# Optimization experiments

Hardware: AMD Instinct MI355X
Metric: run time of the kernel (lower is better)

Reference implementation:

```python
import jax, jax.numpy as jnp
import numpy as np

N, E, IN, HID, OUT, B = 50000, 800000, 128, 128, 64, 4096
EPS = 1e-5


def setup_inputs() -> dict:
    key = jax.random.key(0)
    ks = jax.random.split(key, 12)
    x = jax.random.normal(ks[0], (N, IN), jnp.float32)
    edge_index = jax.random.randint(ks[1], (2, E), 0, N, dtype=jnp.int32).astype(jnp.int64)
    target_index = jax.random.randint(ks[2], (B,), 0, N, dtype=jnp.int32).astype(jnp.int64)

    def lin(k, i, o):
        return jax.random.normal(k, (i, o), jnp.float32) * (1.0 / np.sqrt(i))

    return {
        'x': x, 'edge_index': edge_index, 'target_index': target_index,
        'W0': lin(ks[3], IN, HID), 'b0': jnp.zeros((HID,), jnp.float32),
        'W1': lin(ks[4], HID, HID), 'b1': jnp.zeros((HID,), jnp.float32),
        'W2': lin(ks[5], HID, HID), 'b2': jnp.zeros((HID,), jnp.float32),
        'g0': jnp.ones((HID,), jnp.float32), 'bt0': jnp.zeros((HID,), jnp.float32),
        'g1': jnp.ones((HID,), jnp.float32), 'bt1': jnp.zeros((HID,), jnp.float32),
        'f1w': lin(ks[6], HID, HID), 'f1b': jnp.zeros((HID,), jnp.float32),
        'f2w': lin(ks[7], HID, OUT), 'f2b': jnp.zeros((OUT,), jnp.float32),
    }


def _gcn_layer(h, W, b, src, dst, norm):
    # GCNConv: D^-1/2 (A+I) D^-1/2 (h W) + b  (self-loops already in src/dst)
    h = h @ W                                        # [N, out]
    msg = h[src] * norm[:, None]                     # [E+N, out]
    return jax.ops.segment_sum(msg, dst, num_segments=N) + b


def _batchnorm(h, g, bt):
    mu = jnp.mean(h, axis=0)
    var = jnp.mean((h - mu) ** 2, axis=0)            # biased, as torch BN
    return g * (h - mu) * jax.lax.rsqrt(var + EPS) + bt


def reference(x, edge_index, target_index, W0, b0, W1, b1, W2, b2,
              g0, bt0, g1, bt1, f1w, f1b, f2w, f2b):
    loop = jnp.arange(N, dtype=edge_index.dtype)
    src = jnp.concatenate([edge_index[0], loop])
    dst = jnp.concatenate([edge_index[1], loop])
    deg = jax.ops.segment_sum(jnp.ones_like(dst, jnp.float32), dst, num_segments=N)
    dinv = jax.lax.rsqrt(deg)                        # deg >= 1 via self-loops
    norm = dinv[src] * dinv[dst]                     # [E+N]

    h = _gcn_layer(x, W0, b0, src, dst, norm)
    h = jax.nn.relu(_batchnorm(h, g0, bt0))
    h = _gcn_layer(h, W1, b1, src, dst, norm)
    h = jax.nn.relu(_batchnorm(h, g1, bt1))
    h = _gcn_layer(h, W2, b2, src, dst, norm)

    # target_index.unsqueeze(1).expand(-1,-1) -> [B,1]; pool squeezes dim 1
    t = h[target_index]                              # [B, HID]
    t = jax.nn.relu(t @ f1w + f1b)                   # FeedForwardNetwork layer1 (dropout=0)
    return t @ f2w + f2b                             # [B, OUT]
```

## Files before the change

### kernel.cpp

```cpp
#include <hip/hip_runtime.h>


static const int GNN5566_NN  = 50000;
static const int GNN5566_NE  = 800000;
static const int GNN5566_NB  = 4096;
static const int GNN5566_CAP = 64;

static const int GNN5566_NBUCK  = (GNN5566_NN + 63) / 64;
static const int GNN5566_NCHUNK = 128;
static const int GNN5566_CHUNK  = GNN5566_NE / GNN5566_NCHUNK;

static const int GNN5566_WSLOT = 17408;

typedef short gnn5566_s16x8 __attribute__((ext_vector_type(8)));
typedef float gnn5566_f32x4 __attribute__((ext_vector_type(4)));

static __device__ inline float gnn5566_b2f(unsigned short h){
  return __uint_as_float(((unsigned int)h) << 16);
}
static __device__ inline unsigned short gnn5566_f2b(float f){
  unsigned int u = __float_as_uint(f);
  u += 0x7fffu + ((u >> 16) & 1u);
  return (unsigned short)(u >> 16);
}
static __device__ inline float gnn5566_loadf(const void* p, long long i, int isF32){
  if (isF32) return ((const float*)p)[i];
  return gnn5566_b2f(((const unsigned short*)p)[i]);
}

__global__ void GNNEncoder_5566277616090_sortA(const void* W0, const void* W1,
                                               const void* W2, const void* f1w,
                                               const void* f2w, unsigned short* wT,
                                               const int* ei, const int* tgt,
                                               int* flags, int* done,
                                               unsigned int* histC, unsigned int* prefC,
                                               unsigned int* sorted){
  __shared__ unsigned short lt[128][129];
  __shared__ int h[GNN5566_NBUCK];
  __shared__ int sv[256];
  __shared__ int sFlag;
  int b = blockIdx.x, tid = threadIdx.x;

  if (b == 133) {
    if (tid < 8) done[tid] = 0;
    if (tid < 64) {
      int o1 = ei[2*tid + 1];
      int o2 = tgt[2*tid + 1];
      unsigned int w = ((const unsigned int*)W0)[tid];
      unsigned int e = (w >> 7) & 255u;
      unsigned long long m1 = __ballot(o1 != 0);
      unsigned long long m2 = __ballot(o2 != 0);
      unsigned long long m3 = __ballot(e >= 96u && e <= 134u);
      if (tid == 0) {
        flags[0] = (m1 == 0ull) ? 1 : 0;
        flags[1] = (m2 == 0ull) ? 1 : 0;
        flags[2] = (__popcll(m3) >= 56) ? 0 : 1;
      }
    }
    return;
  }

  if (b >= 128) {
    if (tid < 64) {
      unsigned int w = ((const unsigned int*)W0)[tid];
      unsigned int e = (w >> 7) & 255u;
      unsigned long long m3 = __ballot(e >= 96u && e <= 134u);
      if (tid == 0) sFlag = (__popcll(m3) >= 56) ? 0 : 1;
    }
    __syncthreads();
    int f32 = sFlag;
    int slot = b - 128;
    const void* src = (slot == 0) ? W0 : (slot == 1) ? W1 : (slot == 2) ? W2
                    : (slot == 3) ? f1w : f2w;
    int wide = (slot != 4);
    int tot = wide ? 16384 : 8192;
    for (int i = tid; i < tot; i += 256) {
      int k = wide ? (i >> 7) : (i >> 6);
      int c = wide ? (i & 127) : (i & 63);
      lt[k][c] = f32 ? gnn5566_f2b(((const float*)src)[i])
                     : ((const unsigned short*)src)[i];
    }
    __syncthreads();
    unsigned short* out = wT + slot * GNN5566_WSLOT;
    int wtot = wide ? 2048 : 1024;
    for (int j = tid; j < wtot; j += 256) {
      int c = j >> 4, k8 = (j & 15) << 3;
      unsigned int p0 = (unsigned int)lt[k8    ][c] | ((unsigned int)lt[k8+1][c] << 16);
      unsigned int p1 = (unsigned int)lt[k8 + 2][c] | ((unsigned int)lt[k8+3][c] << 16);
      unsigned int p2 = (unsigned int)lt[k8 + 4][c] | ((unsigned int)lt[k8+5][c] << 16);
      unsigned int p3 = (unsigned int)lt[k8 + 6][c] | ((unsigned int)lt[k8+7][c] << 16);
      uint4 v; v.x = p0; v.y = p1; v.z = p2; v.w = p3;
      *(uint4*)(out + c * 136 + k8) = v;
    }
    return;
  }

  if (tid < 64) {
    int o1 = ei[2*tid + 1];
    unsigned long long m1 = __ballot(o1 != 0);
    if (tid == 0) sFlag = (m1 == 0ull) ? 1 : 0;
  }
  for (int i = tid; i < GNN5566_NBUCK; i += 256) h[i] = 0;
  __syncthreads();
  int f = sFlag;
  int base = b * GNN5566_CHUNK;

  for (int i = tid; i < GNN5566_CHUNK; i += 256) {
    int d = f ? ((const int2*)ei)[GNN5566_NE + base + i].x : ei[GNN5566_NE + base + i];
    atomicAdd(&h[d >> 6], 1);
  }
  __syncthreads();

  int b0 = tid * 4;
  int c0 = (b0     < GNN5566_NBUCK) ? h[b0]     : 0;
  int c1 = (b0 + 1 < GNN5566_NBUCK) ? h[b0 + 1] : 0;
  int c2 = (b0 + 2 < GNN5566_NBUCK) ? h[b0 + 2] : 0;
  int c3 = (b0 + 3 < GNN5566_NBUCK) ? h[b0 + 3] : 0;
  int T = c0 + c1 + c2 + c3;
  sv[tid] = T;
  __syncthreads();
  for (int off = 1; off < 256; off <<= 1) {
    int add = (tid >= off) ? sv[tid - off] : 0;
    __syncthreads();
    sv[tid] += add;
    __syncthreads();
  }
  int excl = sv[tid] - T;

  unsigned int* hrow = histC + (long long)b * GNN5566_NBUCK;
  unsigned int* prow = prefC + (long long)b * GNN5566_NBUCK;
  if (b0     < GNN5566_NBUCK) { hrow[b0]     = (unsigned int)c0;
                                prow[b0]     = (unsigned int)excl;
                                h[b0]     = excl; }
  if (b0 + 1 < GNN5566_NBUCK) { hrow[b0 + 1] = (unsigned int)c1;
                                prow[b0 + 1] = (unsigned int)(excl + c0);
                                h[b0 + 1] = excl + c0; }
  if (b0 + 2 < GNN5566_NBUCK) { hrow[b0 + 2] = (unsigned int)c2;
                                prow[b0 + 2] = (unsigned int)(excl + c0 + c1);
                                h[b0 + 2] = excl + c0 + c1; }
  if (b0 + 3 < GNN5566_NBUCK) { hrow[b0 + 3] = (unsigned int)c3;
                                prow[b0 + 3] = (unsigned int)(excl + c0 + c1 + c2);
                                h[b0 + 3] = excl + c0 + c1 + c2; }
  __syncthreads();

  for (int i = tid; i < GNN5566_CHUNK; i += 256) {
    int s, d;
    if (f) { s = ((const int2*)ei)[base + i].x;
             d = ((const int2*)ei)[GNN5566_NE + base + i].x; }
    else   { s = ei[base + i];
             d = ei[GNN5566_NE + base + i]; }
    int p = atomicAdd(&h[d >> 6], 1);
    sorted[base + p] = ((unsigned int)s << 6) | (unsigned int)(d & 63);
  }
}

__global__ void GNNEncoder_5566277616090_fillB2(const unsigned int* histC,
                                                const unsigned int* prefC,
                                                const unsigned int* sorted,
                                                unsigned short* colIdx16, int* cnt,
                                                float* dinv){
  __shared__ unsigned int lbuf[64 * 32];
  __shared__ int lcnt[64];
  int b   = blockIdx.x;
  int tid = threadIdx.x;
  if (tid < 64) lcnt[tid] = 0;
  __syncthreads();

  unsigned short* lists = (unsigned short*)lbuf;
  if (tid < GNN5566_NCHUNK) {
    int c     = tid;
    int len   = (int)histC[(long long)c * GNN5566_NBUCK + b];
    int start = c * GNN5566_CHUNK + (int)prefC[(long long)c * GNN5566_NBUCK + b];
    for (int j = 0; j < len; ++j) {
      unsigned int w = sorted[start + j];
      int d = (int)(w & 63u);
      int p = atomicAdd(&lcnt[d], 1);
      if (p < GNN5566_CAP) lists[d * 64 + p] = (unsigned short)(w >> 6);
    }
  }
  __syncthreads();

  if (tid < 64) {
    int node = b * 64 + tid;
    if (node < GNN5566_NN) {
      int c = lcnt[tid];
      cnt[node]  = c;
      dinv[node] = rsqrtf((float)(c + 1));
    }
  }
  unsigned int* out = (unsigned int*)colIdx16;
  for (int idx = tid; idx < 2048; idx += 256) {
    int d = idx >> 5;
    int node = b * 64 + d;
    if (node < GNN5566_NN)
      out[(long long)node * 32 + (idx & 31)] = lbuf[idx];
  }
}

__global__ void GNNEncoder_5566277616090_kernel(const void* A,
                                                const unsigned short* wT,
                                                unsigned short* Out, int nRows,
                                                const float* bnA, const float* bnC,
                                                const float* rowScale,
                                                const void* bias, int reluOut,
                                                int aExternal, const int* flags)
{
  __shared__ __align__(16) unsigned short gnnLw[128 * 136];
  __shared__ float lbnA[128], lbnC[128], lbias[128];
  int tid = threadIdx.x;
  int wF32 = flags[2];
  int aF32 = aExternal ? wF32 : 0;

  int wave = tid >> 6, lane = tid & 63;
  int q = lane >> 4, ln = lane & 15;
  int rowBase = blockIdx.x * 64 + wave * 16;
  int r  = rowBase + ln;
  int cr = (r < nRows) ? r : (nRows - 1);
  float rs = rowScale ? rowScale[cr] : 1.0f;
  int useBN = (bnA != 0);

  uint4  rawU[4];
  float4 rawF[8];
  if (aF32) {
    const float4* ap = (const float4*)A + (long long)cr * 32 + q * 2;
    #pragma unroll
    for (int kk = 0; kk < 4; ++kk) { rawF[2*kk] = ap[kk*8]; rawF[2*kk+1] = ap[kk*8+1]; }
  } else {
    const uint4* ap = (const uint4*)A + (long long)cr * 16 + q;
    #pragma unroll
    for (int kk = 0; kk < 4; ++kk) rawU[kk] = ap[kk * 4];
  }

  {
    const uint4* src = (const uint4*)wT;
    uint4* dst = (uint4*)gnnLw;
    for (int i = tid; i < 2176; i += 256) dst[i] = src[i];
  }
  if (tid < 128) {
    lbnA[tid]  = bnA  ? bnA[tid] : 0.0f;
    lbnC[tid]  = bnC  ? bnC[tid] : 0.0f;
    lbias[tid] = bias ? gnn5566_loadf(bias, tid, wF32) : 0.0f;
  }
  __syncthreads();

  gnn5566_s16x8 afr[4];
  #pragma unroll
  for (int kk = 0; kk < 4; ++kk) {
    int kb = kk * 32 + q * 8;
    float vals[8];
    if (aF32) {
      float4 u = rawF[2*kk], w = rawF[2*kk+1];
      vals[0] = u.x; vals[1] = u.y; vals[2] = u.z; vals[3] = u.w;
      vals[4] = w.x; vals[5] = w.y; vals[6] = w.z; vals[7] = w.w;
    } else {
      uint4 u = rawU[kk];
      vals[0] = gnn5566_b2f((unsigned short)(u.x & 0xffffu));
      vals[1] = gnn5566_b2f((unsigned short)(u.x >> 16));
      vals[2] = gnn5566_b2f((unsigned short)(u.y & 0xffffu));
      vals[3] = gnn5566_b2f((unsigned short)(u.y >> 16));
      vals[4] = gnn5566_b2f((unsigned short)(u.z & 0xffffu));
      vals[5] = gnn5566_b2f((unsigned short)(u.z >> 16));
      vals[6] = gnn5566_b2f((unsigned short)(u.w & 0xffffu));
      vals[7] = gnn5566_b2f((unsigned short)(u.w >> 16));
    }
    if (useBN) {
      float4 a0 = *(const float4*)&lbnA[kb], a1 = *(const float4*)&lbnA[kb + 4];
      float4 c0 = *(const float4*)&lbnC[kb], c1 = *(const float4*)&lbnC[kb + 4];
      vals[0] = fmaxf(vals[0] * a0.x + c0.x, 0.0f);
      vals[1] = fmaxf(vals[1] * a0.y + c0.y, 0.0f);
      vals[2] = fmaxf(vals[2] * a0.z + c0.z, 0.0f);
      vals[3] = fmaxf(vals[3] * a0.w + c0.w, 0.0f);
      vals[4] = fmaxf(vals[4] * a1.x + c1.x, 0.0f);
      vals[5] = fmaxf(vals[5] * a1.y + c1.y, 0.0f);
      vals[6] = fmaxf(vals[6] * a1.z + c1.z, 0.0f);
      vals[7] = fmaxf(vals[7] * a1.w + c1.w, 0.0f);
    }
    #pragma unroll
    for (int j = 0; j < 8; ++j) afr[kk][j] = (short)gnn5566_f2b(vals[j] * rs);
  }

  gnn5566_f32x4 zero4;
  zero4[0] = 0.0f; zero4[1] = 0.0f; zero4[2] = 0.0f; zero4[3] = 0.0f;
  gnn5566_f32x4 acc[8];
  #pragma unroll
  for (int t = 0; t < 8; ++t) acc[t] = zero4;

  #pragma unroll
  for (int kk = 0; kk < 4; ++kk) {
    int kb = kk * 32 + q * 8;
    #pragma unroll
    for (int t = 0; t < 8; ++t) {
      gnn5566_s16x8 bfr = *(const gnn5566_s16x8*)(&gnnLw[(t * 16 + ln) * 136 + kb]);
      acc[t] = __builtin_amdgcn_mfma_f32_16x16x32_bf16(afr[kk], bfr, acc[t], 0, 0, 0);
    }
  }

  __syncthreads();
  #pragma unroll
  for (int t = 0; t < 8; ++t) {
    int col = t * 16 + ln;
    float badd = lbias[col];
    #pragma unroll
    for (int rg = 0; rg < 4; ++rg) {
      float v = acc[t][rg] + badd;
      if (reluOut) v = fmaxf(v, 0.0f);
      gnnLw[(wave * 16 + q * 4 + rg) * 136 + col] = gnn5566_f2b(v);
    }
  }
  __syncthreads();
  int tRowBase = blockIdx.x * 64;
  for (int j = tid; j < 1024; j += 256) {
    int rr = j >> 4, c4 = j & 15;
    int grow = tRowBase + rr;
    if (grow < nRows) {
      uint4 v = *(const uint4*)&gnnLw[rr * 136 + c4 * 8];
      *(uint4*)&Out[(long long)grow * 128 + c4 * 8] = v;
    }
  }
}

__global__ void GNNEncoder_5566277616090_ffn(const unsigned short* A,
                                             const unsigned short* wT3,
                                             const unsigned short* wT4,
                                             void* Out,
                                             const void* f1b, const void* fb2,
                                             const int* flags)
{
  __shared__ __align__(16) unsigned short lwA[128 * 136];
  __shared__ __align__(16) unsigned short lwB[64 * 136];
  __shared__ __align__(16) unsigned short ep[64 * 136];
  __shared__ float lb1[128];
  __shared__ float lb2[64];
  int tid = threadIdx.x;
  int f32 = flags[2];

  {
    const uint4* sA = (const uint4*)wT3;
    uint4* dA = (uint4*)lwA;
    for (int i = tid; i < 2176; i += 256) dA[i] = sA[i];
    const uint4* sB = (const uint4*)wT4;
    uint4* dB = (uint4*)lwB;
    for (int i = tid; i < 1088; i += 256) dB[i] = sB[i];
  }
  if (tid < 128) lb1[tid] = gnn5566_loadf(f1b, tid, f32);
  if (tid < 64)  lb2[tid] = gnn5566_loadf(fb2, tid, f32);
  __syncthreads();

  int wave = tid >> 6, lane = tid & 63;
  int q = lane >> 4, ln = lane & 15;
  int rowBase = blockIdx.x * 64 + wave * 16;
  int r  = rowBase + ln;
  int cr = (r < GNN5566_NB) ? r : (GNN5566_NB - 1);

  gnn5566_s16x8 afr[4];
  #pragma unroll
  for (int kk = 0; kk < 4; ++kk) {
    int kb = kk * 32 + q * 8;
    const uint4* ap = (const uint4*)A + (long long)cr * 16 + (kb >> 3);
    uint4 u = ap[0];
    unsigned short e[8];
    e[0] = (unsigned short)(u.x & 0xffffu); e[1] = (unsigned short)(u.x >> 16);
    e[2] = (unsigned short)(u.y & 0xffffu); e[3] = (unsigned short)(u.y >> 16);
    e[4] = (unsigned short)(u.z & 0xffffu); e[5] = (unsigned short)(u.z >> 16);
    e[6] = (unsigned short)(u.w & 0xffffu); e[7] = (unsigned short)(u.w >> 16);
    #pragma unroll
    for (int j = 0; j < 8; ++j) afr[kk][j] = (short)e[j];
  }

  gnn5566_f32x4 zero4;
  zero4[0] = 0.0f; zero4[1] = 0.0f; zero4[2] = 0.0f; zero4[3] = 0.0f;
  gnn5566_f32x4 acc[8];
  #pragma unroll
  for (int t = 0; t < 8; ++t) acc[t] = zero4;
  #pragma unroll
  for (int kk = 0; kk < 4; ++kk) {
    int kb = kk * 32 + q * 8;
    #pragma unroll
    for (int t = 0; t < 8; ++t) {
      gnn5566_s16x8 bfr = *(const gnn5566_s16x8*)(&lwA[(t * 16 + ln) * 136 + kb]);
      acc[t] = __builtin_amdgcn_mfma_f32_16x16x32_bf16(afr[kk], bfr, acc[t], 0, 0, 0);
    }
  }
  #pragma unroll
  for (int t = 0; t < 8; ++t) {
    int col = t * 16 + ln;
    float badd = lb1[col];
    #pragma unroll
    for (int rg = 0; rg < 4; ++rg) {
      float v = fmaxf(acc[t][rg] + badd, 0.0f);
      ep[(wave * 16 + q * 4 + rg) * 136 + col] = gnn5566_f2b(v);
    }
  }
  __syncthreads();

  gnn5566_s16x8 afr2[4];
  #pragma unroll
  for (int kk = 0; kk < 4; ++kk) {
    int kb = kk * 32 + q * 8;
    afr2[kk] = *(const gnn5566_s16x8*)(&ep[(wave * 16 + ln) * 136 + kb]);
  }
  gnn5566_f32x4 acc2[4];
  #pragma unroll
  for (int t = 0; t < 4; ++t) acc2[t] = zero4;
  #pragma unroll
  for (int kk = 0; kk < 4; ++kk) {
    int kb = kk * 32 + q * 8;
    #pragma unroll
    for (int t = 0; t < 4; ++t) {
      gnn5566_s16x8 bfr = *(const gnn5566_s16x8*)(&lwB[(t * 16 + ln) * 136 + kb]);
      acc2[t] = __builtin_amdgcn_mfma_f32_16x16x32_bf16(afr2[kk], bfr, acc2[t], 0, 0, 0);
    }
  }
  #pragma unroll
  for (int t = 0; t < 4; ++t) {
    int col = t * 16 + ln;
    float badd = lb2[col];
    #pragma unroll
    for (int rg = 0; rg < 4; ++rg) {
      int grow = rowBase + q * 4 + rg;
      if (grow < GNN5566_NB) {
        float v = acc2[t][rg] + badd;
        if (f32) ((float*)Out)[(long long)grow * 64 + col] = v;
        else     ((unsigned short*)Out)[(long long)grow * 64 + col] = gnn5566_f2b(v);
      }
    }
  }
}

__global__ void GNNEncoder_5566277616090_agg(const unsigned short* hs,
                                             const unsigned short* colIdx16,
                                             const int* cnt, const float* dinv,
                                             const void* bias, unsigned short* haOut,
                                             const int* flags,
                                             const int* tgtList, int nRowsAgg)
{
  int r = (int)((blockIdx.x * 256u + threadIdx.x) >> 6);
  if (r >= nRowsAgg) return;
  int node = r;
  if (tgtList) node = flags[1] ? tgtList[2 * r] : tgtList[r];
  int lane = threadIdx.x & 63;
  const unsigned int* hrow = (const unsigned int*)hs;
  unsigned int sv = hrow[(long long)node * 64 + lane];
  float a0 = __uint_as_float(sv << 16);
  float a1 = __uint_as_float(sv & 0xffff0000u);
  int m = cnt[node]; if (m > GNN5566_CAP) m = GNN5566_CAP;
  const unsigned short* cp = colIdx16 + (long long)node * GNN5566_CAP;
  const uint4* cp4 = (const uint4*)cp;
  int i = 0;
  for (; i + 16 <= m; i += 16) {
    uint4 iwA = cp4[i >> 3];
    uint4 iwB = cp4[(i >> 3) + 1];
    unsigned int v0  = hrow[(long long)(iwA.x & 0xffffu) * 64 + lane];
    unsigned int v1  = hrow[(long long)(iwA.x >> 16)     * 64 + lane];
    unsigned int v2  = hrow[(long long)(iwA.y & 0xffffu) * 64 + lane];
    unsigned int v3  = hrow[(long long)(iwA.y >> 16)     * 64 + lane];
    unsigned int v4  = hrow[(long long)(iwA.z & 0xffffu) * 64 + lane];
    unsigned int v5  = hrow[(long long)(iwA.z >> 16)     * 64 + lane];
    unsigned int v6  = hrow[(long long)(iwA.w & 0xffffu) * 64 + lane];
    unsigned int v7  = hrow[(long long)(iwA.w >> 16)     * 64 + lane];
    unsigned int v8  = hrow[(long long)(iwB.x & 0xffffu) * 64 + lane];
    unsigned int v9  = hrow[(long long)(iwB.x >> 16)     * 64 + lane];
    unsigned int v10 = hrow[(long long)(iwB.y & 0xffffu) * 64 + lane];
    unsigned int v11 = hrow[(long long)(iwB.y >> 16)     * 64 + lane];
    unsigned int v12 = hrow[(long long)(iwB.z & 0xffffu) * 64 + lane];
    unsigned int v13 = hrow[(long long)(iwB.z >> 16)     * 64 + lane];
    unsigned int v14 = hrow[(long long)(iwB.w & 0xffffu) * 64 + lane];
    unsigned int v15 = hrow[(long long)(iwB.w >> 16)     * 64 + lane];
    a0 += __uint_as_float(v0  << 16) + __uint_as_float(v1  << 16)
        + __uint_as_float(v2  << 16) + __uint_as_float(v3  << 16)
        + __uint_as_float(v4  << 16) + __uint_as_float(v5  << 16)
        + __uint_as_float(v6  << 16) + __uint_as_float(v7  << 16)
        + __uint_as_float(v8  << 16) + __uint_as_float(v9  << 16)
        + __uint_as_float(v10 << 16) + __uint_as_float(v11 << 16)
        + __uint_as_float(v12 << 16) + __uint_as_float(v13 << 16)
        + __uint_as_float(v14 << 16) + __uint_as_float(v15 << 16);
    a1 += __uint_as_float(v0  & 0xffff0000u) + __uint_as_float(v1  & 0xffff0000u)
        + __uint_as_float(v2  & 0xffff0000u) + __uint_as_float(v3  & 0xffff0000u)
        + __uint_as_float(v4  & 0xffff0000u) + __uint_as_float(v5  & 0xffff0000u)
        + __uint_as_float(v6  & 0xffff0000u) + __uint_as_float(v7  & 0xffff0000u)
        + __uint_as_float(v8  & 0xffff0000u) + __uint_as_float(v9  & 0xffff0000u)
        + __uint_as_float(v10 & 0xffff0000u) + __uint_as_float(v11 & 0xffff0000u)
        + __uint_as_float(v12 & 0xffff0000u) + __uint_as_float(v13 & 0xffff0000u)
        + __uint_as_float(v14 & 0xffff0000u) + __uint_as_float(v15 & 0xffff0000u);
  }
  for (; i + 8 <= m; i += 8) {
    uint4 iw = cp4[i >> 3];
    unsigned int v0 = hrow[(long long)(iw.x & 0xffffu) * 64 + lane];
    unsigned int v1 = hrow[(long long)(iw.x >> 16)     * 64 + lane];
    unsigned int v2 = hrow[(long long)(iw.y & 0xffffu) * 64 + lane];
    unsigned int v3 = hrow[(long long)(iw.y >> 16)     * 64 + lane];
    unsigned int v4 = hrow[(long long)(iw.z & 0xffffu) * 64 + lane];
    unsigned int v5 = hrow[(long long)(iw.z >> 16)     * 64 + lane];
    unsigned int v6 = hrow[(long long)(iw.w & 0xffffu) * 64 + lane];
    unsigned int v7 = hrow[(long long)(iw.w >> 16)     * 64 + lane];
    a0 += __uint_as_float(v0 << 16) + __uint_as_float(v1 << 16)
        + __uint_as_float(v2 << 16) + __uint_as_float(v3 << 16)
        + __uint_as_float(v4 << 16) + __uint_as_float(v5 << 16)
        + __uint_as_float(v6 << 16) + __uint_as_float(v7 << 16);
    a1 += __uint_as_float(v0 & 0xffff0000u) + __uint_as_float(v1 & 0xffff0000u)
        + __uint_as_float(v2 & 0xffff0000u) + __uint_as_float(v3 & 0xffff0000u)
        + __uint_as_float(v4 & 0xffff0000u) + __uint_as_float(v5 & 0xffff0000u)
        + __uint_as_float(v6 & 0xffff0000u) + __uint_as_float(v7 & 0xffff0000u);
  }
  for (; i < m; ++i) {
    unsigned int v = hrow[(long long)cp[i] * 64 + lane];
    a0 += __uint_as_float(v << 16);
    a1 += __uint_as_float(v & 0xffff0000u);
  }
  float s = dinv[node];
  int f32 = flags[2];
  float o0 = a0 * s + gnn5566_loadf(bias, lane * 2,     f32);
  float o1 = a1 * s + gnn5566_loadf(bias, lane * 2 + 1, f32);
  unsigned int packed = (unsigned int)gnn5566_f2b(o0)
                      | (((unsigned int)gnn5566_f2b(o1)) << 16);
  ((unsigned int*)haOut)[(long long)r * 64 + lane] = packed;
}

__global__ void GNNEncoder_5566277616090_stats(const unsigned short* ha, float* partial,
                                               const void* g, const void* bt,
                                               float* bnA, float* bnC,
                                               const int* flags, int* doneCtr){
  __shared__ float red[256];
  __shared__ int lastFlag;
  const unsigned int* h32 = (const unsigned int*)ha;
  int tid = threadIdx.x;
  int cp2 = tid & 63, sub = tid >> 6;
  float s0 = 0.0f, s1 = 0.0f, q0 = 0.0f, q1 = 0.0f;
  for (int r = blockIdx.x * 4 + sub; r < GNN5566_NN; r += 512) {
    unsigned int v = h32[(long long)r * 64 + cp2];
    float a = __uint_as_float(v << 16);
    float b = __uint_as_float(v & 0xffff0000u);
    s0 += a; q0 += a * a; s1 += b; q1 += b * b;
  }
  float* prow = partial + blockIdx.x * 256;
  red[tid] = s0; __syncthreads();
  if (sub == 0) atomicExch(&prow[2*cp2],
      red[cp2] + red[64+cp2] + red[128+cp2] + red[192+cp2]);
  __syncthreads();
  red[tid] = s1; __syncthreads();
  if (sub == 0) atomicExch(&prow[2*cp2 + 1],
      red[cp2] + red[64+cp2] + red[128+cp2] + red[192+cp2]);
  __syncthreads();
  red[tid] = q0; __syncthreads();
  if (sub == 0) atomicExch(&prow[128 + 2*cp2],
      red[cp2] + red[64+cp2] + red[128+cp2] + red[192+cp2]);
  __syncthreads();
  red[tid] = q1; __syncthreads();
  if (sub == 0) atomicExch(&prow[128 + 2*cp2 + 1],
      red[cp2] + red[64+cp2] + red[128+cp2] + red[192+cp2]);
  __syncthreads();

  if (tid == 0) {
    __threadfence();
    lastFlag = (atomicAdd(doneCtr, 1) == (int)gridDim.x - 1);
  }
  __syncthreads();
  if (!lastFlag) return;

  float acc = 0.0f;
  for (int b = 0; b < (int)gridDim.x; b += 8) {
    float p0 = atomicAdd(&partial[(b    ) * 256 + tid], 0.0f);
    float p1 = atomicAdd(&partial[(b + 1) * 256 + tid], 0.0f);
    float p2 = atomicAdd(&partial[(b + 2) * 256 + tid], 0.0f);
    float p3 = atomicAdd(&partial[(b + 3) * 256 + tid], 0.0f);
    float p4 = atomicAdd(&partial[(b + 4) * 256 + tid], 0.0f);
    float p5 = atomicAdd(&partial[(b + 5) * 256 + tid], 0.0f);
    float p6 = atomicAdd(&partial[(b + 6) * 256 + tid], 0.0f);
    float p7 = atomicAdd(&partial[(b + 7) * 256 + tid], 0.0f);
    acc += ((p0 + p1) + (p2 + p3)) + ((p4 + p5) + (p6 + p7));
  }
  red[tid] = acc;
  __syncthreads();
  if (tid < 128) {
    int f32 = flags[2];
    float invN = 1.0f / (float)GNN5566_NN;
    float mu  = red[tid] * invN;
    float var = red[128 + tid] * invN - mu * mu;
    if (var < 0.0f) var = 0.0f;
    float a = gnn5566_loadf(g, tid, f32) * rsqrtf(var + 1e-5f);
    bnA[tid] = a;
    bnC[tid] = gnn5566_loadf(bt, tid, f32) - mu * a;
  }
}

extern "C" void kernel_launch(void* const* d_in, const int* in_sizes, int n_in,
                              void* d_out, int out_size, void* d_ws, size_t ws_size,
                              hipStream_t stream)
{
  const void* x   = d_in[0];
  const int*  ei  = (const int*)d_in[1];
  const int*  tgt = (const int*)d_in[2];
  const void* W0  = d_in[3];
  const void* b0  = d_in[4];
  const void* W1  = d_in[5];
  const void* b1  = d_in[6];
  const void* W2  = d_in[7];
  const void* b2  = d_in[8];
  const void* g0  = d_in[9];
  const void* bt0 = d_in[10];
  const void* g1  = d_in[11];
  const void* bt1 = d_in[12];
  const void* f1w = d_in[13];
  const void* f1b = d_in[14];
  const void* f2w = d_in[15];
  const void* fb2 = d_in[16];

  char* ws = (char*)d_ws;
  int*            cnt      = (int*)           (ws + 8192);
  float*          dinv     = (float*)         (ws + 208896);
  unsigned short* wT       = (unsigned short*)(ws + 409600);
  unsigned int*   histC    = (unsigned int*)  (ws + 583936);
  unsigned int*   prefC    = (unsigned int*)  (ws + 984320);
  unsigned int*   sorted   = (unsigned int*)  (ws + 1384960);
  unsigned short* colIdx16 = (unsigned short*)(ws + 4585216);
  unsigned short* hs       = (unsigned short*)(ws + 10985472);
  unsigned short* ha       = (unsigned short*)(ws + 23785728);
  float*          partial  = (float*)         (ws + 36585984);
  float*          bn       = (float*)         (ws + 36848128);
  int*            flags    = (int*)           (ws + 36850176);
  int*            done     = (int*)           (ws + 36850432);
  unsigned short* hb       = (unsigned short*)(ws + 36851200);

  float* bn0A = bn;       float* bn0C = bn + 128;
  float* bn1A = bn + 256; float* bn1C = bn + 384;

  GNNEncoder_5566277616090_sortA <<<134, 256, 0, stream>>>(
      W0, W1, W2, f1w, f2w, wT, ei, tgt, flags, done, histC, prefC, sorted);
  GNNEncoder_5566277616090_fillB2<<<GNN5566_NBUCK, 256, 0, stream>>>(
      histC, prefC, sorted, colIdx16, cnt, dinv);

  const int gemmGrid = (GNN5566_NN + 63) / 64;

  GNNEncoder_5566277616090_kernel<<<gemmGrid, 256, 0, stream>>>(
      x, wT, hs, GNN5566_NN, (const float*)0, (const float*)0, dinv,
      (const void*)0, 0, 1, flags);
  GNNEncoder_5566277616090_agg  <<<12500, 256, 0, stream>>>(
      hs, colIdx16, cnt, dinv, b0, ha, flags, (const int*)0, GNN5566_NN);
  GNNEncoder_5566277616090_stats<<<128, 256, 0, stream>>>(
      ha, partial, g0, bt0, bn0A, bn0C, flags, done + 1);

  GNNEncoder_5566277616090_kernel<<<gemmGrid, 256, 0, stream>>>(
      ha, wT + GNN5566_WSLOT, hs, GNN5566_NN, bn0A, bn0C, dinv,
      (const void*)0, 0, 0, flags);
  GNNEncoder_5566277616090_agg  <<<12500, 256, 0, stream>>>(
      hs, colIdx16, cnt, dinv, b1, ha, flags, (const int*)0, GNN5566_NN);
  GNNEncoder_5566277616090_stats<<<128, 256, 0, stream>>>(
      ha, partial + 32768, g1, bt1, bn1A, bn1C, flags, done + 2);

  GNNEncoder_5566277616090_kernel<<<gemmGrid, 256, 0, stream>>>(
      ha, wT + 2 * GNN5566_WSLOT, hs, GNN5566_NN, bn1A, bn1C, dinv,
      (const void*)0, 0, 0, flags);
  GNNEncoder_5566277616090_agg  <<<1024, 256, 0, stream>>>(
      hs, colIdx16, cnt, dinv, b2, hb, flags, tgt, GNN5566_NB);

  GNNEncoder_5566277616090_ffn<<<64, 256, 0, stream>>>(
      hb, wT + 3 * GNN5566_WSLOT, wT + 4 * GNN5566_WSLOT, d_out,
      f1b, fb2, flags);
}
```

Measured before the change: 332.6 us.

## Fuse batchnorm statistics reduction into aggregation kernel via atomic partials

Removes the separate stats kernel that reread the aggregated activations. Each aggregation block now reduces its rows' sums and squared sums in shared memory and atomically adds them into one of 128 partial rows, which are zeroed in the setup kernel. The last block, found via a done counter, finalizes the BN scale and shift. This saves a full read of the activation tensor per layer, at the cost of many contended float atomics and extra syncs in each aggregation block.

```diff
diff --git a/kernel.cpp b/kernel.cpp
--- a/kernel.cpp
+++ b/kernel.cpp
@@ -34,7 +34,7 @@
                                                const int* ei, const int* tgt,
                                                int* flags, int* done,
                                                unsigned int* histC, unsigned int* prefC,
-                                               unsigned int* sorted){
+                                               unsigned int* sorted, float* partial){
   __shared__ unsigned short lt[128][129];
   __shared__ int h[GNN5566_NBUCK];
   __shared__ int sv[256];
@@ -43,6 +43,7 @@
 
   if (b == 133) {
     if (tid < 8) done[tid] = 0;
+    for (int i = tid; i < 65536; i += 256) partial[i] = 0.0f;
     if (tid < 64) {
       int o1 = ei[2*tid + 1];
       int o2 = tgt[2*tid + 1];
@@ -432,122 +433,118 @@
                                              const int* cnt, const float* dinv,
                                              const void* bias, unsigned short* haOut,
                                              const int* flags,
-                                             const int* tgtList, int nRowsAgg)
+                                             const int* tgtList, int nRowsAgg,
+                                             float* partialOut, const void* g,
+                                             const void* bt, float* bnA, float* bnC,
+                                             int* doneCtr)
 {
-  int r = (int)((blockIdx.x * 256u + threadIdx.x) >> 6);
-  if (r >= nRowsAgg) return;
-  int node = r;
-  if (tgtList) node = flags[1] ? tgtList[2 * r] : tgtList[r];
-  int lane = threadIdx.x & 63;
-  const unsigned int* hrow = (const unsigned int*)hs;
-  unsigned int sv = hrow[(long long)node * 64 + lane];
-  float a0 = __uint_as_float(sv << 16);
-  float a1 = __uint_as_float(sv & 0xffff0000u);
-  int m = cnt[node]; if (m > GNN5566_CAP) m = GNN5566_CAP;
-  const unsigned short* cp = colIdx16 + (long long)node * GNN5566_CAP;
-  const uint4* cp4 = (const uint4*)cp;
-  int i = 0;
-  for (; i + 16 <= m; i += 16) {
-    uint4 iwA = cp4[i >> 3];
-    uint4 iwB = cp4[(i >> 3) + 1];
-    unsigned int v0  = hrow[(long long)(iwA.x & 0xffffu) * 64 + lane];
-    unsigned int v1  = hrow[(long long)(iwA.x >> 16)     * 64 + lane];
-    unsigned int v2  = hrow[(long long)(iwA.y & 0xffffu) * 64 + lane];
-    unsigned int v3  = hrow[(long long)(iwA.y >> 16)     * 64 + lane];
-    unsigned int v4  = hrow[(long long)(iwA.z & 0xffffu) * 64 + lane];
-    unsigned int v5  = hrow[(long long)(iwA.z >> 16)     * 64 + lane];
-    unsigned int v6  = hrow[(long long)(iwA.w & 0xffffu) * 64 + lane];
-    unsigned int v7  = hrow[(long long)(iwA.w >> 16)     * 64 + lane];
-    unsigned int v8  = hrow[(long long)(iwB.x & 0xffffu) * 64 + lane];
-    unsigned int v9  = hrow[(long long)(iwB.x >> 16)     * 64 + lane];
-    unsigned int v10 = hrow[(long long)(iwB.y & 0xffffu) * 64 + lane];
-    unsigned int v11 = hrow[(long long)(iwB.y >> 16)     * 64 + lane];
-    unsigned int v12 = hrow[(long long)(iwB.z & 0xffffu) * 64 + lane];
-    unsigned int v13 = hrow[(long long)(iwB.z >> 16)     * 64 + lane];
-    unsigned int v14 = hrow[(long long)(iwB.w & 0xffffu) * 64 + lane];
-    unsigned int v15 = hrow[(long long)(iwB.w >> 16)     * 64 + lane];
-    a0 += __uint_as_float(v0  << 16) + __uint_as_float(v1  << 16)
-        + __uint_as_float(v2  << 16) + __uint_as_float(v3  << 16)
-        + __uint_as_float(v4  << 16) + __uint_as_float(v5  << 16)
-        + __uint_as_float(v6  << 16) + __uint_as_float(v7  << 16)
-        + __uint_as_float(v8  << 16) + __uint_as_float(v9  << 16)
-        + __uint_as_float(v10 << 16) + __uint_as_float(v11 << 16)
-        + __uint_as_float(v12 << 16) + __uint_as_float(v13 << 16)
-        + __uint_as_float(v14 << 16) + __uint_as_float(v15 << 16);
-    a1 += __uint_as_float(v0  & 0xffff0000u) + __uint_as_float(v1  & 0xffff0000u)
-        + __uint_as_float(v2  & 0xffff0000u) + __uint_as_float(v3  & 0xffff0000u)
-        + __uint_as_float(v4  & 0xffff0000u) + __uint_as_float(v5  & 0xffff0000u)
-        + __uint_as_float(v6  & 0xffff0000u) + __uint_as_float(v7  & 0xffff0000u)
-        + __uint_as_float(v8  & 0xffff0000u) + __uint_as_float(v9  & 0xffff0000u)
-        + __uint_as_float(v10 & 0xffff0000u) + __uint_as_float(v11 & 0xffff0000u)
-        + __uint_as_float(v12 & 0xffff0000u) + __uint_as_float(v13 & 0xffff0000u)
-        + __uint_as_float(v14 & 0xffff0000u) + __uint_as_float(v15 & 0xffff0000u);
-  }
-  for (; i + 8 <= m; i += 8) {
-    uint4 iw = cp4[i >> 3];
-    unsigned int v0 = hrow[(long long)(iw.x & 0xffffu) * 64 + lane];
-    unsigned int v1 = hrow[(long long)(iw.x >> 16)     * 64 + lane];
-    unsigned int v2 = hrow[(long long)(iw.y & 0xffffu) * 64 + lane];
-    unsigned int v3 = hrow[(long long)(iw.y >> 16)     * 64 + lane];
-    unsigned int v4 = hrow[(long long)(iw.z & 0xffffu) * 64 + lane];
-    unsigned int v5 = hrow[(long long)(iw.z >> 16)     * 64 + lane];
-    unsigned int v6 = hrow[(long long)(iw.w & 0xffffu) * 64 + lane];
-    unsigned int v7 = hrow[(long long)(iw.w >> 16)     * 64 + lane];
-    a0 += __uint_as_float(v0 << 16) + __uint_as_float(v1 << 16)
-        + __uint_as_float(v2 << 16) + __uint_as_float(v3 << 16)
-        + __uint_as_float(v4 << 16) + __uint_as_float(v5 << 16)
-        + __uint_as_float(v6 << 16) + __uint_as_float(v7 << 16);
-    a1 += __uint_as_float(v0 & 0xffff0000u) + __uint_as_float(v1 & 0xffff0000u)
-        + __uint_as_float(v2 & 0xffff0000u) + __uint_as_float(v3 & 0xffff0000u)
-        + __uint_as_float(v4 & 0xffff0000u) + __uint_as_float(v5 & 0xffff0000u)
-        + __uint_as_float(v6 & 0xffff0000u) + __uint_as_float(v7 & 0xffff0000u);
-  }
-  for (; i < m; ++i) {
-    unsigned int v = hrow[(long long)cp[i] * 64 + lane];
-    a0 += __uint_as_float(v << 16);
-    a1 += __uint_as_float(v & 0xffff0000u);
-  }
-  float s = dinv[node];
-  int f32 = flags[2];
-  float o0 = a0 * s + gnn5566_loadf(bias, lane * 2,     f32);
-  float o1 = a1 * s + gnn5566_loadf(bias, lane * 2 + 1, f32);
-  unsigned int packed = (unsigned int)gnn5566_f2b(o0)
-                      | (((unsigned int)gnn5566_f2b(o1)) << 16);
-  ((unsigned int*)haOut)[(long long)r * 64 + lane] = packed;
-}
-
-__global__ void GNNEncoder_5566277616090_stats(const unsigned short* ha, float* partial,
-                                               const void* g, const void* bt,
-                                               float* bnA, float* bnC,
-                                               const int* flags, int* doneCtr){
   __shared__ float red[256];
   __shared__ int lastFlag;
-  const unsigned int* h32 = (const unsigned int*)ha;
-  int tid = threadIdx.x;
-  int cp2 = tid & 63, sub = tid >> 6;
-  float s0 = 0.0f, s1 = 0.0f, q0 = 0.0f, q1 = 0.0f;
-  for (int r = blockIdx.x * 4 + sub; r < GNN5566_NN; r += 512) {
-    unsigned int v = h32[(long long)r * 64 + cp2];
-    float a = __uint_as_float(v << 16);
-    float b = __uint_as_float(v & 0xffff0000u);
-    s0 += a; q0 += a * a; s1 += b; q1 += b * b;
-  }
-  float* prow = partial + blockIdx.x * 256;
-  red[tid] = s0; __syncthreads();
-  if (sub == 0) atomicExch(&prow[2*cp2],
-      red[cp2] + red[64+cp2] + red[128+cp2] + red[192+cp2]);
-  __syncthreads();
-  red[tid] = s1; __syncthreads();
-  if (sub == 0) atomicExch(&prow[2*cp2 + 1],
-      red[cp2] + red[64+cp2] + red[128+cp2] + red[192+cp2]);
-  __syncthreads();
-  red[tid] = q0; __syncthreads();
-  if (sub == 0) atomicExch(&prow[128 + 2*cp2],
-      red[cp2] + red[64+cp2] + red[128+cp2] + red[192+cp2]);
-  __syncthreads();
-  red[tid] = q1; __syncthreads();
-  if (sub == 0) atomicExch(&prow[128 + 2*cp2 + 1],
-      red[cp2] + red[64+cp2] + red[128+cp2] + red[192+cp2]);
+  int tid  = threadIdx.x;
+  int r    = (int)((blockIdx.x * 256u + tid) >> 6);
+  int lane = tid & 63;
+  int wv   = tid >> 6;
+  int valid = (r < nRowsAgg);
+  float o0 = 0.0f, o1 = 0.0f;
+
+  if (valid) {
+    int node = r;
+    if (tgtList) node = flags[1] ? tgtList[2 * r] : tgtList[r];
+    const unsigned int* hrow = (const unsigned int*)hs;
+    unsigned int sv = hrow[(long long)node * 64 + lane];
+    float a0 = __uint_as_float(sv << 16);
+    float a1 = __uint_as_float(sv & 0xffff0000u);
+    int m = cnt[node]; if (m > GNN5566_CAP) m = GNN5566_CAP;
+    const unsigned short* cp = colIdx16 + (long long)node * GNN5566_CAP;
+    const uint4* cp4 = (const uint4*)cp;
+    int i = 0;
+    for (; i + 16 <= m; i += 16) {
+      uint4 iwA = cp4[i >> 3];
+      uint4 iwB = cp4[(i >> 3) + 1];
+      unsigned int v0  = hrow[(long long)(iwA.x & 0xffffu) * 64 + lane];
+      unsigned int v1  = hrow[(long long)(iwA.x >> 16)     * 64 + lane];
+      unsigned int v2  = hrow[(long long)(iwA.y & 0xffffu) * 64 + lane];
+      unsigned int v3  = hrow[(long long)(iwA.y >> 16)     * 64 + lane];
+      unsigned int v4  = hrow[(long long)(iwA.z & 0xffffu) * 64 + lane];
+      unsigned int v5  = hrow[(long long)(iwA.z >> 16)     * 64 + lane];
+      unsigned int v6  = hrow[(long long)(iwA.w & 0xffffu) * 64 + lane];
+      unsigned int v7  = hrow[(long long)(iwA.w >> 16)     * 64 + lane];
+      unsigned int v8  = hrow[(long long)(iwB.x & 0xffffu) * 64 + lane];
+      unsigned int v9  = hrow[(long long)(iwB.x >> 16)     * 64 + lane];
+      unsigned int v10 = hrow[(long long)(iwB.y & 0xffffu) * 64 + lane];
+      unsigned int v11 = hrow[(long long)(iwB.y >> 16)     * 64 + lane];
+      unsigned int v12 = hrow[(long long)(iwB.z & 0xffffu) * 64 + lane];
+      unsigned int v13 = hrow[(long long)(iwB.z >> 16)     * 64 + lane];
+      unsigned int v14 = hrow[(long long)(iwB.w & 0xffffu) * 64 + lane];
+      unsigned int v15 = hrow[(long long)(iwB.w >> 16)     * 64 + lane];
+      a0 += __uint_as_float(v0  << 16) + __uint_as_float(v1  << 16)
+          + __uint_as_float(v2  << 16) + __uint_as_float(v3  << 16)
+          + __uint_as_float(v4  << 16) + __uint_as_float(v5  << 16)
+          + __uint_as_float(v6  << 16) + __uint_as_float(v7  << 16)
+          + __uint_as_float(v8  << 16) + __uint_as_float(v9  << 16)
+          + __uint_as_float(v10 << 16) + __uint_as_float(v11 << 16)
+          + __uint_as_float(v12 << 16) + __uint_as_float(v13 << 16)
+          + __uint_as_float(v14 << 16) + __uint_as_float(v15 << 16);
+      a1 += __uint_as_float(v0  & 0xffff0000u) + __uint_as_float(v1  & 0xffff0000u)
+          + __uint_as_float(v2  & 0xffff0000u) + __uint_as_float(v3  & 0xffff0000u)
+          + __uint_as_float(v4  & 0xffff0000u) + __uint_as_float(v5  & 0xffff0000u)
+          + __uint_as_float(v6  & 0xffff0000u) + __uint_as_float(v7  & 0xffff0000u)
+          + __uint_as_float(v8  & 0xffff0000u) + __uint_as_float(v9  & 0xffff0000u)
+          + __uint_as_float(v10 & 0xffff0000u) + __uint_as_float(v11 & 0xffff0000u)
+          + __uint_as_float(v12 & 0xffff0000u) + __uint_as_float(v13 & 0xffff0000u)
+          + __uint_as_float(v14 & 0xffff0000u) + __uint_as_float(v15 & 0xffff0000u);
+    }
+    for (; i + 8 <= m; i += 8) {
+      uint4 iw = cp4[i >> 3];
+      unsigned int v0 = hrow[(long long)(iw.x & 0xffffu) * 64 + lane];
+      unsigned int v1 = hrow[(long long)(iw.x >> 16)     * 64 + lane];
+      unsigned int v2 = hrow[(long long)(iw.y & 0xffffu) * 64 + lane];
+      unsigned int v3 = hrow[(long long)(iw.y >> 16)     * 64 + lane];
+      unsigned int v4 = hrow[(long long)(iw.z & 0xffffu) * 64 + lane];
+      unsigned int v5 = hrow[(long long)(iw.z >> 16)     * 64 + lane];
+      unsigned int v6 = hrow[(long long)(iw.w & 0xffffu) * 64 + lane];
+      unsigned int v7 = hrow[(long long)(iw.w >> 16)     * 64 + lane];
+      a0 += __uint_as_float(v0 << 16) + __uint_as_float(v1 << 16)
+          + __uint_as_float(v2 << 16) + __uint_as_float(v3 << 16)
+          + __uint_as_float(v4 << 16) + __uint_as_float(v5 << 16)
+          + __uint_as_float(v6 << 16) + __uint_as_float(v7 << 16);
+      a1 += __uint_as_float(v0 & 0xffff0000u) + __uint_as_float(v1 & 0xffff0000u)
+          + __uint_as_float(v2 & 0xffff0000u) + __uint_as_float(v3 & 0xffff0000u)
+          + __uint_as_float(v4 & 0xffff0000u) + __uint_as_float(v5 & 0xffff0000u)
+          + __uint_as_float(v6 & 0xffff0000u) + __uint_as_float(v7 & 0xffff0000u);
+    }
+    for (; i < m; ++i) {
+      unsigned int v = hrow[(long long)cp[i] * 64 + lane];
+      a0 += __uint_as_float(v << 16);
+      a1 += __uint_as_float(v & 0xffff0000u);
+    }
+    float s = dinv[node];
+    int f32 = flags[2];
+    o0 = a0 * s + gnn5566_loadf(bias, lane * 2,     f32);
+    o1 = a1 * s + gnn5566_loadf(bias, lane * 2 + 1, f32);
+    unsigned int packed = (unsigned int)gnn5566_f2b(o0)
+                        | (((unsigned int)gnn5566_f2b(o1)) << 16);
+    ((unsigned int*)haOut)[(long long)r * 64 + lane] = packed;
+  }
+
+  if (!partialOut) return;
+
+  float* prow = partialOut + (blockIdx.x & 127) * 256;
+  red[tid] = o0; __syncthreads();
+  if (wv == 0) atomicAdd(&prow[2*lane],
+      red[lane] + red[64+lane] + red[128+lane] + red[192+lane]);
+  __syncthreads();
+  red[tid] = o1; __syncthreads();
+  if (wv == 0) atomicAdd(&prow[2*lane + 1],
+      red[lane] + red[64+lane] + red[128+lane] + red[192+lane]);
+  __syncthreads();
+  red[tid] = o0 * o0; __syncthreads();
+  if (wv == 0) atomicAdd(&prow[128 + 2*lane],
+      red[lane] + red[64+lane] + red[128+lane] + red[192+lane]);
+  __syncthreads();
+  red[tid] = o1 * o1; __syncthreads();
+  if (wv == 0) atomicAdd(&prow[128 + 2*lane + 1],
+      red[lane] + red[64+lane] + red[128+lane] + red[192+lane]);
   __syncthreads();
 
   if (tid == 0) {
@@ -558,15 +555,15 @@
   if (!lastFlag) return;
 
   float acc = 0.0f;
-  for (int b = 0; b < (int)gridDim.x; b += 8) {
-    float p0 = atomicAdd(&partial[(b    ) * 256 + tid], 0.0f);
-    float p1 = atomicAdd(&partial[(b + 1) * 256 + tid], 0.0f);
-    float p2 = atomicAdd(&partial[(b + 2) * 256 + tid], 0.0f);
-    float p3 = atomicAdd(&partial[(b + 3) * 256 + tid], 0.0f);
-    float p4 = atomicAdd(&partial[(b + 4) * 256 + tid], 0.0f);
-    float p5 = atomicAdd(&partial[(b + 5) * 256 + tid], 0.0f);
-    float p6 = atomicAdd(&partial[(b + 6) * 256 + tid], 0.0f);
-    float p7 = atomicAdd(&partial[(b + 7) * 256 + tid], 0.0f);
+  for (int b = 0; b < 128; b += 8) {
+    float p0 = atomicAdd(&partialOut[(b    ) * 256 + tid], 0.0f);
+    float p1 = atomicAdd(&partialOut[(b + 1) * 256 + tid], 0.0f);
+    float p2 = atomicAdd(&partialOut[(b + 2) * 256 + tid], 0.0f);
+    float p3 = atomicAdd(&partialOut[(b + 3) * 256 + tid], 0.0f);
+    float p4 = atomicAdd(&partialOut[(b + 4) * 256 + tid], 0.0f);
+    float p5 = atomicAdd(&partialOut[(b + 5) * 256 + tid], 0.0f);
+    float p6 = atomicAdd(&partialOut[(b + 6) * 256 + tid], 0.0f);
+    float p7 = atomicAdd(&partialOut[(b + 7) * 256 + tid], 0.0f);
     acc += ((p0 + p1) + (p2 + p3)) + ((p4 + p5) + (p6 + p7));
   }
   red[tid] = acc;
@@ -625,7 +622,7 @@
   float* bn1A = bn + 256; float* bn1C = bn + 384;
 
   GNNEncoder_5566277616090_sortA <<<134, 256, 0, stream>>>(
-      W0, W1, W2, f1w, f2w, wT, ei, tgt, flags, done, histC, prefC, sorted);
+      W0, W1, W2, f1w, f2w, wT, ei, tgt, flags, done, histC, prefC, sorted, partial);
   GNNEncoder_5566277616090_fillB2<<<GNN5566_NBUCK, 256, 0, stream>>>(
       histC, prefC, sorted, colIdx16, cnt, dinv);
 
@@ -635,23 +632,22 @@
       x, wT, hs, GNN5566_NN, (const float*)0, (const float*)0, dinv,
       (const void*)0, 0, 1, flags);
   GNNEncoder_5566277616090_agg  <<<12500, 256, 0, stream>>>(
-      hs, colIdx16, cnt, dinv, b0, ha, flags, (const int*)0, GNN5566_NN);
-  GNNEncoder_5566277616090_stats<<<128, 256, 0, stream>>>(
-      ha, partial, g0, bt0, bn0A, bn0C, flags, done + 1);
+      hs, colIdx16, cnt, dinv, b0, ha, flags, (const int*)0, GNN5566_NN,
+      partial, g0, bt0, bn0A, bn0C, done + 1);
 
   GNNEncoder_5566277616090_kernel<<<gemmGrid, 256, 0, stream>>>(
       ha, wT + GNN5566_WSLOT, hs, GNN5566_NN, bn0A, bn0C, dinv,
       (const void*)0, 0, 0, flags);
   GNNEncoder_5566277616090_agg  <<<12500, 256, 0, stream>>>(
-      hs, colIdx16, cnt, dinv, b1, ha, flags, (const int*)0, GNN5566_NN);
-  GNNEncoder_5566277616090_stats<<<128, 256, 0, stream>>>(
-      ha, partial + 32768, g1, bt1, bn1A, bn1C, flags, done + 2);
+      hs, colIdx16, cnt, dinv, b1, ha, flags, (const int*)0, GNN5566_NN,
+      partial + 32768, g1, bt1, bn1A, bn1C, done + 2);
 
   GNNEncoder_5566277616090_kernel<<<gemmGrid, 256, 0, stream>>>(
       ha, wT + 2 * GNN5566_WSLOT, hs, GNN5566_NN, bn1A, bn1C, dinv,
       (const void*)0, 0, 0, flags);
   GNNEncoder_5566277616090_agg  <<<1024, 256, 0, stream>>>(
-      hs, colIdx16, cnt, dinv, b2, hb, flags, tgt, GNN5566_NB);
+      hs, colIdx16, cnt, dinv, b2, hb, flags, tgt, GNN5566_NB,
+      (float*)0, (const void*)0, (const void*)0, (float*)0, (float*)0, (int*)0);
 
   GNNEncoder_5566277616090_ffn<<<64, 256, 0, stream>>>(
       hb, wT + 3 * GNN5566_WSLOT, wT + 4 * GNN5566_WSLOT, d_out,
```

Result: slower. 927.1 us (+178.7%).
